# Performance work log

Hardware: AMD Instinct MI355X
Metric: run time of the kernel (lower is better)

The kernel has to match this reference:

```python
import jax, jax.numpy as jnp
import numpy as np

NB_STEPS = 50  # quadrature steps (51 Clenshaw-Curtis nodes)
IN_D = 8
HIDDEN = [256, 256, 256]
B = 8192


def _cc_quadrature(nb_steps):
    # Clenshaw-Curtis weights/nodes, exactly as in UMNN's ParallelNeuralIntegral
    lam = np.arange(nb_steps + 1).reshape(-1, 1)
    lam = np.cos((lam @ lam.T) * np.pi / nb_steps)
    lam[:, 0] = 0.5
    lam[:, -1] = 0.5 * lam[:, -1]
    lam = lam * 2.0 / nb_steps
    W = np.arange(nb_steps + 1).reshape(-1, 1)
    W[np.arange(1, nb_steps + 1, 2)] = 0
    W = 2.0 / (1 - W.astype(np.float64) ** 2)
    W[0] = 1.0
    W[np.arange(1, nb_steps + 1, 2)] = 0.0
    cc_weights = (lam.T @ W).astype(np.float32)  # [S+1, 1]
    steps = np.cos(np.arange(nb_steps + 1).reshape(-1, 1) * np.pi / nb_steps).astype(np.float32)  # [S+1,1]
    return jnp.asarray(cc_weights), jnp.asarray(steps)


def setup_inputs() -> dict:
    key = jax.random.key(0)
    ks = jax.random.split(key, 20)
    inp = {
        "x": jax.random.normal(ks[0], (B, 1), dtype=jnp.float32),
        "h": jax.random.normal(ks[1], (B, IN_D - 1), dtype=jnp.float32),
    }
    # integrand net: in_d -> 256 -> 256 -> 256 -> 1
    i_dims = [IN_D] + HIDDEN + [1]
    for li, (d0, d1) in enumerate(zip(i_dims, i_dims[1:])):
        scale = 1.0 / np.sqrt(d0)
        inp[f"iW{li}"] = jax.random.uniform(ks[2 + li], (d0, d1), jnp.float32, -scale, scale)
        inp[f"ib{li}"] = jax.random.uniform(ks[6 + li], (d1,), jnp.float32, -scale, scale)
    # h net: (in_d-1) -> 256 -> 256 -> 256 -> 2
    h_dims = [IN_D - 1] + HIDDEN + [2]
    for li, (d0, d1) in enumerate(zip(h_dims, h_dims[1:])):
        scale = 1.0 / np.sqrt(d0)
        inp[f"hW{li}"] = jax.random.uniform(ks[10 + li], (d0, d1), jnp.float32, -scale, scale)
        inp[f"hb{li}"] = jax.random.uniform(ks[14 + li], (d1,), jnp.float32, -scale, scale)
    return inp


def _integrand(z, Ws, bs):
    # IntegrandNN: Linear+ReLU chain, final Linear+ELU, then +1
    for W, b in zip(Ws[:-1], bs[:-1]):
        z = jax.nn.relu(z @ W + b)
    return jax.nn.elu(z @ Ws[-1] + bs[-1]) + 1.0


def _hnet(z, Ws, bs):
    # Linear+ReLU chain, final Linear (ReLU popped)
    for W, b in zip(Ws[:-1], bs[:-1]):
        z = jax.nn.relu(z @ W + b)
    return z @ Ws[-1] + bs[-1]


def _forward(x, h, iWs, ibs, hWs, hbs):
    cc_w, steps = _cc_quadrature(NB_STEPS)  # [S,1], [S,1]
    S = NB_STEPS + 1
    b = x.shape[0]
    # quadrature nodes mapped from [-1,1] to [0, x] (x0 = 0)
    X = x[:, None, :] * (steps[None, :, :] + 1.0) * 0.5          # [B,S,1]
    Hs = jnp.broadcast_to(h[:, None, :], (b, S, h.shape[1]))     # [B,S,in_d-1]
    z = jnp.concatenate([X, Hs], axis=-1)                        # [B,S,in_d]
    dz = _integrand(z, iWs, ibs)                                 # [B,S,1]
    integral = jnp.sum(dz * cc_w[None, :, :], axis=1) * x * 0.5  # [B,1]
    out = _hnet(h, hWs, hbs)                                     # [B,2]
    offset = out[:, :1]
    scaling = jnp.exp(out[:, 1:2])
    return scaling * integral + offset


def reference(x, h, iW0, ib0, iW1, ib1, iW2, ib2, iW3, ib3,
              hW0, hb0, hW1, hb1, hW2, hb2, hW3, hb3):
    iWs = [iW0, iW1, iW2, iW3]
    ibs = [ib0, ib1, ib2, ib3]
    hWs = [hW0, hW1, hW2, hW3]
    hbs = [hb0, hb1, hb2, hb3]
    return _forward(x, h, iWs, ibs, hWs, hbs)
```

## Files before the change

### kernel.cpp

```cpp
#include <hip/hip_runtime.h>
#include <hip/hip_bf16.h>
#include <math.h>

using bf16x8 = __attribute__((ext_vector_type(8))) __bf16;
using f32x4  = __attribute__((ext_vector_type(4))) float;

#define B_SZ    8192
#define S_STEPS 51
#define M_ROWS  (B_SZ * S_STEPS)
#define TROWS   128

__device__ __forceinline__ f32x4 mfma16(bf16x8 a, bf16x8 b, f32x4 c) {
    return __builtin_amdgcn_mfma_f32_16x16x32_bf16(a, b, c, 0, 0, 0);
}

__global__ void ccq_kernel(float* __restrict__ ccw, float* __restrict__ stp) {
    int s = threadIdx.x;
    if (s >= S_STEPS) return;
    double pi50 = M_PI / 50.0;
    double acc = 0.0;
    for (int j = 0; j <= 50; j += 2) {
        double wq = (j == 0) ? 1.0 : 2.0 / (1.0 - (double)(j * j));
        double m;
        if (s == 0) m = 0.5;
        else if (s == 50) m = 0.5;
        else m = cos((double)(j * s) * pi50);
        acc += m * wq;
    }
    ccw[s] = (float)(acc * (2.0 / 50.0));
    stp[s] = (float)cos((double)s * pi50);
}

struct PackArgs {
    const float* src[8];
    __hip_bfloat16* dst[8];
    int Ks[8], Ns[8], KST[8], perm[8];
    int prefix[9];
};

__global__ void pack_all(PackArgs pa) {
    int idx = blockIdx.x * 256 + threadIdx.x;
    if (idx >= pa.prefix[8]) return;
    int m = 0;
    while (idx >= pa.prefix[m + 1]) ++m;
    int e = idx - pa.prefix[m];
    int KSTEPS = pa.KST[m];
    int j    = e & 7;
    int lane = (e >> 3) & 63;
    int ks   = (e >> 9) % KSTEPS;
    int cg   = (e >> 9) / KSTEPS;
    int col = cg * 16 + (lane & 15);
    int k   = ks * 32 + (lane >> 4) * 8 + j;
    int kk  = pa.perm[m] ? ((k & ~31) + ((k & 31) >> 1) + (k & 1) * 16) : k;
    float v = (kk < pa.Ks[m] && col < pa.Ns[m]) ? pa.src[m][kk * pa.Ns[m] + col] : 0.0f;
    ((__bf16*)pa.dst[m])[e] = (__bf16)v;
}


template<int KSTEPS, int CHUNKS, int MASK>
__device__ __forceinline__ void gemm_compute(const __bf16* __restrict__ actIn,
                                             const __bf16* __restrict__ wpack,
                                             f32x4 (&acc)[4][4],
                                             int wr, int wc, int lane) {
    const bf16x8* wp = (const bf16x8*)wpack;
    const int la = lane & 15, hi = lane >> 4;

#pragma unroll
    for (int ks = 0; ks < KSTEPS; ++ks) {
        bf16x8 bbuf[4];
#pragma unroll
        for (int n = 0; n < 4; ++n)
            bbuf[n] = wp[((wc * 4 + n) * KSTEPS + ks) * 64 + lane];
#pragma unroll
        for (int m = 0; m < 4; ++m) {
            int row   = wr * 64 + m * 16 + la;
            int chunk = ks * 4 + hi;
            bf16x8 af = *(const bf16x8*)(actIn + (row * CHUNKS + (chunk ^ (row & MASK))) * 8);
#pragma unroll
            for (int n = 0; n < 4; ++n)
                acc[m][n] = mfma16(af, bbuf[n], acc[m][n]);
        }
    }
}

__device__ __forceinline__ void epilogue_store(f32x4 (&acc)[4][4],
                                               const float* __restrict__ bias,
                                               __bf16* __restrict__ actOut,
                                               int wr, int wc, int lane) {
    const int la = lane & 15, hi = lane >> 4;
    unsigned* dst = (unsigned*)actOut;
#pragma unroll
    for (int p = 0; p < 2; ++p) {
        int f0 = wc * 64 + p * 32 + la;
        float b0 = bias[f0], b1 = bias[f0 + 16];
        int kd = (wc * 2 + p) * 16 + la;
#pragma unroll
        for (int m = 0; m < 4; ++m) {
#pragma unroll
            for (int r = 0; r < 4; ++r) {
                int row = wr * 64 + m * 16 + hi * 4 + r;
                float v0 = fmaxf(acc[m][2 * p][r] + b0, 0.0f);
                float v1 = fmaxf(acc[m][2 * p + 1][r] + b1, 0.0f);
                union { __bf16 h[2]; unsigned u; } cv;
                cv.h[0] = (__bf16)v0; cv.h[1] = (__bf16)v1;
                dst[(row * 32 + ((kd >> 2) ^ (row & 7))) * 4 + (kd & 3)] = cv.u;
            }
        }
    }
}

template<int MODE>
__device__ __forceinline__ void final_layer(const __bf16* __restrict__ actIn,
                                            const __bf16* __restrict__ wpack,
                                            const float* __restrict__ bias,
                                            float* __restrict__ out0,
                                            float* __restrict__ out1,
                                            int rb, int wid, int lane) {
    const bf16x8* wp = (const bf16x8*)wpack;
    f32x4 acc = (f32x4)0.0f;
    for (int ks = 0; ks < 8; ++ks) {
        int row   = wid * 16 + (lane & 15);
        int chunk = ks * 4 + (lane >> 4);
        bf16x8 af = *(const bf16x8*)(actIn + (row * 32 + (chunk ^ (row & 7))) * 8);
        acc = mfma16(af, wp[ks * 64 + lane], acc);
    }
    int col = lane & 15;
    if (MODE == 0) {
        if (col == 0) {
            float b = bias[0];
#pragma unroll
            for (int r = 0; r < 4; ++r) {
                int row = wid * 16 + (lane >> 4) * 4 + r;
                float v = acc[r] + b;
                out0[rb + row] = (v > 0.0f) ? (v + 1.0f) : expf(v);
            }
        }
    } else {
        if (col < 2) {
            float b = bias[col];
            float* dst = (col == 0) ? out0 : out1;
#pragma unroll
            for (int r = 0; r < 4; ++r) {
                int row = wid * 16 + (lane >> 4) * 4 + r;
                dst[rb + row] = acc[r] + b;
            }
        }
    }
}

template<int MODE>
__global__ __launch_bounds__(512, 2) void mlp_kernel(
    const float* __restrict__ x, const float* __restrict__ h,
    const float* __restrict__ steps,
    const __bf16* __restrict__ w0p, const __bf16* __restrict__ w1p,
    const __bf16* __restrict__ w2p, const __bf16* __restrict__ w3p,
    const float* __restrict__ b0, const float* __restrict__ b1,
    const float* __restrict__ b2, const float* __restrict__ b3,
    float* __restrict__ out0, float* __restrict__ out1) {
    __shared__ __bf16 act[TROWS * 256];
    __shared__ __bf16 zin[TROWS * 32];

    int tid  = threadIdx.x;
    int lane = tid & 63;
    int wid  = tid >> 6;
    int wr   = wid >> 2;
    int wc   = wid & 3;
    int rb   = blockIdx.x * TROWS;

    {
        int row   = tid >> 2;
        int cpart = tid & 3;
        float vals[8];
        if (MODE == 0) {
            int s  = rb >> 13;
            int i  = (rb & (B_SZ - 1)) + row;
            float sc = (steps[s] + 1.0f) * 0.5f;
#pragma unroll
            for (int j = 0; j < 8; ++j) {
                int c = cpart * 8 + j;
                float v = 0.0f;
                if (c == 0) v = x[i] * sc;
                else if (c < 8) v = h[i * 7 + c - 1];
                vals[j] = v;
            }
        } else {
            int i = rb + row;
#pragma unroll
            for (int j = 0; j < 8; ++j) {
                int c = cpart * 8 + j;
                vals[j] = (c < 7) ? h[i * 7 + c] : 0.0f;
            }
        }
        bf16x8 zv;
#pragma unroll
        for (int j = 0; j < 8; ++j) zv[j] = (__bf16)vals[j];
        int zidx = (row * 4 + (cpart ^ (row & 3))) * 8;
        *(bf16x8*)(zin + zidx) = zv;
    }
    __syncthreads();

    f32x4 acc[4][4];

#pragma unroll
    for (int m = 0; m < 4; ++m)
#pragma unroll
        for (int n = 0; n < 4; ++n) acc[m][n] = (f32x4)0.0f;
    gemm_compute<1, 4, 3>(zin, w0p, acc, wr, wc, lane);
    epilogue_store(acc, b0, act, wr, wc, lane);
    __syncthreads();

#pragma unroll
    for (int m = 0; m < 4; ++m)
#pragma unroll
        for (int n = 0; n < 4; ++n) acc[m][n] = (f32x4)0.0f;
    gemm_compute<8, 32, 7>(act, w1p, acc, wr, wc, lane);
    __syncthreads();
    epilogue_store(acc, b1, act, wr, wc, lane);
    __syncthreads();

#pragma unroll
    for (int m = 0; m < 4; ++m)
#pragma unroll
        for (int n = 0; n < 4; ++n) acc[m][n] = (f32x4)0.0f;
    gemm_compute<8, 32, 7>(act, w2p, acc, wr, wc, lane);
    __syncthreads();
    epilogue_store(acc, b2, act, wr, wc, lane);
    __syncthreads();

    final_layer<MODE>(act, w3p, b3, out0, out1, rb, wid, lane);
}

__global__ void reduce_kernel(const float* __restrict__ dz, const float* __restrict__ x,
                              const float* __restrict__ ho, const float* __restrict__ hs,
                              const float* __restrict__ ccw, float* __restrict__ out) {
    __shared__ float w[S_STEPS];
    int t = threadIdx.x;
    if (t < S_STEPS) w[t] = ccw[t];
    __syncthreads();
    int i = blockIdx.x * blockDim.x + t;
    float acc = 0.0f;
    for (int s = 0; s < S_STEPS; ++s) acc += dz[s * B_SZ + i] * w[s];
    float integral = acc * x[i] * 0.5f;
    out[i] = expf(hs[i]) * integral + ho[i];
}

extern "C" void kernel_launch(void* const* d_in, const int* in_sizes, int n_in,
                              void* d_out, int out_size, void* d_ws, size_t ws_size,
                              hipStream_t stream) {
    (void)in_sizes; (void)n_in; (void)out_size; (void)ws_size;
    const float* x = (const float*)d_in[0];
    const float* h = (const float*)d_in[1];
    const float* iW[4] = {(const float*)d_in[2], (const float*)d_in[4],
                          (const float*)d_in[6], (const float*)d_in[8]};
    const float* ib[4] = {(const float*)d_in[3], (const float*)d_in[5],
                          (const float*)d_in[7], (const float*)d_in[9]};
    const float* hW[4] = {(const float*)d_in[10], (const float*)d_in[12],
                          (const float*)d_in[14], (const float*)d_in[16]};
    const float* hb[4] = {(const float*)d_in[11], (const float*)d_in[13],
                          (const float*)d_in[15], (const float*)d_in[17]};

    size_t off = 0;
    auto alloc = [&](size_t bytes) -> void* {
        void* p = (char*)d_ws + off;
        off += (bytes + 255) & ~(size_t)255;
        return p;
    };
    float*  dz   = (float*)alloc((size_t)M_ROWS * 4);
    float*  ho   = (float*)alloc(B_SZ * 4);
    float*  hs   = (float*)alloc(B_SZ * 4);
    float*  ccw  = (float*)alloc(64 * 4);
    float*  stp  = (float*)alloc(64 * 4);
    __bf16* iW0p = (__bf16*)alloc(16 * 1 * 512 * 2);
    __bf16* iW1p = (__bf16*)alloc(16 * 8 * 512 * 2);
    __bf16* iW2p = (__bf16*)alloc(16 * 8 * 512 * 2);
    __bf16* iW3p = (__bf16*)alloc(1 * 8 * 512 * 2);
    __bf16* hW0p = (__bf16*)alloc(16 * 1 * 512 * 2);
    __bf16* hW1p = (__bf16*)alloc(16 * 8 * 512 * 2);
    __bf16* hW2p = (__bf16*)alloc(16 * 8 * 512 * 2);
    __bf16* hW3p = (__bf16*)alloc(1 * 8 * 512 * 2);

    ccq_kernel<<<1, 64, 0, stream>>>(ccw, stp);

    PackArgs pa;
    const float* srcs[8] = {iW[0], iW[1], iW[2], iW[3], hW[0], hW[1], hW[2], hW[3]};
    __bf16*      dsts[8] = {iW0p, iW1p, iW2p, iW3p, hW0p, hW1p, hW2p, hW3p};
    int Ks[8]  = {8, 256, 256, 256, 7, 256, 256, 256};
    int Ns[8]  = {256, 256, 256, 1, 256, 256, 256, 2};
    int KST[8] = {1, 8, 8, 8, 1, 8, 8, 8};
    int CG[8]  = {16, 16, 16, 1, 16, 16, 16, 1};
    int PM[8]  = {0, 1, 1, 1, 0, 1, 1, 1};
    int pfx = 0;
    for (int m = 0; m < 8; ++m) {
        pa.src[m] = srcs[m];
        pa.dst[m] = (__hip_bfloat16*)dsts[m];
        pa.Ks[m] = Ks[m]; pa.Ns[m] = Ns[m]; pa.KST[m] = KST[m]; pa.perm[m] = PM[m];
        pa.prefix[m] = pfx;
        pfx += CG[m] * KST[m] * 512;
    }
    pa.prefix[8] = pfx;
    pack_all<<<(pfx + 255) / 256, 256, 0, stream>>>(pa);

    mlp_kernel<0><<<M_ROWS / TROWS, 512, 0, stream>>>(
        x, h, stp, iW0p, iW1p, iW2p, iW3p, ib[0], ib[1], ib[2], ib[3], dz, dz);
    mlp_kernel<1><<<B_SZ / TROWS, 512, 0, stream>>>(
        x, h, stp, hW0p, hW1p, hW2p, hW3p, hb[0], hb[1], hb[2], hb[3], ho, hs);

    reduce_kernel<<<B_SZ / 256, 256, 0, stream>>>(dz, x, ho, hs, ccw, (float*)d_out);
}
```

Before: 174.8 us.

## Switch MLP GEMMs to 32x32x16 MFMA with 64-row tiles and 4 waves

Replaces the 16x16x32 bf16 MFMA tiling with 32x32x16 MFMA and shrinks the row tile from 128 to 64 rows per block, using 256 threads instead of 512. Each wave now owns a 64x64 output tile as 2x2 32x32 accumulators. The weight packing, epilogue layout and final layer are reworked to match the new MFMA operand and accumulator layouts. The aim is fewer MFMA issues and a better instruction mix per output. In exchange, only two of the four waves do the final-layer work, and launch bounds change to allow four blocks per CU.

```diff
diff --git a/kernel.cpp b/kernel.cpp
--- a/kernel.cpp
+++ b/kernel.cpp
@@ -3,15 +3,15 @@
 #include <math.h>
 
 using bf16x8 = __attribute__((ext_vector_type(8))) __bf16;
-using f32x4  = __attribute__((ext_vector_type(4))) float;
+using f32x16 = __attribute__((ext_vector_type(16))) float;
 
 #define B_SZ    8192
 #define S_STEPS 51
 #define M_ROWS  (B_SZ * S_STEPS)
-#define TROWS   128
-
-__device__ __forceinline__ f32x4 mfma16(bf16x8 a, bf16x8 b, f32x4 c) {
-    return __builtin_amdgcn_mfma_f32_16x16x32_bf16(a, b, c, 0, 0, 0);
+#define TROWS   64
+
+__device__ __forceinline__ f32x16 mfma32(bf16x8 a, bf16x8 b, f32x16 c) {
+    return __builtin_amdgcn_mfma_f32_32x32x16_bf16(a, b, c, 0, 0, 0);
 }
 
 __global__ void ccq_kernel(float* __restrict__ ccw, float* __restrict__ stp) {
@@ -44,67 +44,61 @@
     int m = 0;
     while (idx >= pa.prefix[m + 1]) ++m;
     int e = idx - pa.prefix[m];
-    int KSTEPS = pa.KST[m];
+    int KST = pa.KST[m];
     int j    = e & 7;
     int lane = (e >> 3) & 63;
-    int ks   = (e >> 9) % KSTEPS;
-    int cg   = (e >> 9) / KSTEPS;
-    int col = cg * 16 + (lane & 15);
-    int k   = ks * 32 + (lane >> 4) * 8 + j;
-    int kk  = pa.perm[m] ? ((k & ~31) + ((k & 31) >> 1) + (k & 1) * 16) : k;
+    int ks   = (e >> 9) % KST;
+    int cg   = (e >> 9) / KST;
+    int col = cg * 32 + (lane & 31);
+    int k   = ks * 16 + (lane >> 5) * 8 + j;
+    int kk  = pa.perm[m] ? ((k & ~63) | (((k & 63) >> 1) + 32 * (k & 1))) : k;
     float v = (kk < pa.Ks[m] && col < pa.Ns[m]) ? pa.src[m][kk * pa.Ns[m] + col] : 0.0f;
     ((__bf16*)pa.dst[m])[e] = (__bf16)v;
 }
 
 
-template<int KSTEPS, int CHUNKS, int MASK>
+template<int KST, int CHUNKS, int MASK>
 __device__ __forceinline__ void gemm_compute(const __bf16* __restrict__ actIn,
                                              const __bf16* __restrict__ wpack,
-                                             f32x4 (&acc)[4][4],
-                                             int wr, int wc, int lane) {
+                                             f32x16 (&acc)[2][2],
+                                             int wc, int lane) {
     const bf16x8* wp = (const bf16x8*)wpack;
-    const int la = lane & 15, hi = lane >> 4;
-
-#pragma unroll
-    for (int ks = 0; ks < KSTEPS; ++ks) {
-        bf16x8 bbuf[4];
-#pragma unroll
-        for (int n = 0; n < 4; ++n)
-            bbuf[n] = wp[((wc * 4 + n) * KSTEPS + ks) * 64 + lane];
-#pragma unroll
-        for (int m = 0; m < 4; ++m) {
-            int row   = wr * 64 + m * 16 + la;
-            int chunk = ks * 4 + hi;
+    const int la = lane & 31, hi = lane >> 5;
+#pragma unroll 4
+    for (int ks = 0; ks < KST; ++ks) {
+        bf16x8 b0 = wp[((wc * 2 + 0) * KST + ks) * 64 + lane];
+        bf16x8 b1 = wp[((wc * 2 + 1) * KST + ks) * 64 + lane];
+        int chunk = ks * 2 + hi;
+#pragma unroll
+        for (int m = 0; m < 2; ++m) {
+            int row = m * 32 + la;
             bf16x8 af = *(const bf16x8*)(actIn + (row * CHUNKS + (chunk ^ (row & MASK))) * 8);
-#pragma unroll
-            for (int n = 0; n < 4; ++n)
-                acc[m][n] = mfma16(af, bbuf[n], acc[m][n]);
-        }
-    }
-}
-
-__device__ __forceinline__ void epilogue_store(f32x4 (&acc)[4][4],
+            acc[m][0] = mfma32(af, b0, acc[m][0]);
+            acc[m][1] = mfma32(af, b1, acc[m][1]);
+        }
+    }
+}
+
+__device__ __forceinline__ void epilogue_store(f32x16 (&acc)[2][2],
                                                const float* __restrict__ bias,
                                                __bf16* __restrict__ actOut,
-                                               int wr, int wc, int lane) {
-    const int la = lane & 15, hi = lane >> 4;
+                                               int wc, int lane) {
+    const int la = lane & 31, hi = lane >> 5;
     unsigned* dst = (unsigned*)actOut;
-#pragma unroll
-    for (int p = 0; p < 2; ++p) {
-        int f0 = wc * 64 + p * 32 + la;
-        float b0 = bias[f0], b1 = bias[f0 + 16];
-        int kd = (wc * 2 + p) * 16 + la;
-#pragma unroll
-        for (int m = 0; m < 4; ++m) {
-#pragma unroll
-            for (int r = 0; r < 4; ++r) {
-                int row = wr * 64 + m * 16 + hi * 4 + r;
-                float v0 = fmaxf(acc[m][2 * p][r] + b0, 0.0f);
-                float v1 = fmaxf(acc[m][2 * p + 1][r] + b1, 0.0f);
-                union { __bf16 h[2]; unsigned u; } cv;
-                cv.h[0] = (__bf16)v0; cv.h[1] = (__bf16)v1;
-                dst[(row * 32 + ((kd >> 2) ^ (row & 7))) * 4 + (kd & 3)] = cv.u;
-            }
+    int F = wc * 64 + la;
+    float b0 = bias[F], b1 = bias[F + 32];
+    int d = wc * 32 + la;
+    int c = d >> 2, w = d & 3;
+#pragma unroll
+    for (int m = 0; m < 2; ++m) {
+#pragma unroll
+        for (int r = 0; r < 16; ++r) {
+            int row = m * 32 + (r & 3) + 8 * (r >> 2) + 4 * hi;
+            float v0 = fmaxf(acc[m][0][r] + b0, 0.0f);
+            float v1 = fmaxf(acc[m][1][r] + b1, 0.0f);
+            union { __bf16 h2[2]; unsigned u; } cv;
+            cv.h2[0] = (__bf16)v0; cv.h2[1] = (__bf16)v1;
+            dst[(row * 32 + (c ^ (row & 7))) * 4 + w] = cv.u;
         }
     }
 }
@@ -117,39 +111,40 @@
                                             float* __restrict__ out1,
                                             int rb, int wid, int lane) {
     const bf16x8* wp = (const bf16x8*)wpack;
-    f32x4 acc = (f32x4)0.0f;
-    for (int ks = 0; ks < 8; ++ks) {
-        int row   = wid * 16 + (lane & 15);
-        int chunk = ks * 4 + (lane >> 4);
+    const int la = lane & 31, hi = lane >> 5;
+    f32x16 acc = (f32x16)0.0f;
+    int row = wid * 32 + la;
+#pragma unroll 4
+    for (int ks = 0; ks < 16; ++ks) {
+        int chunk = ks * 2 + hi;
         bf16x8 af = *(const bf16x8*)(actIn + (row * 32 + (chunk ^ (row & 7))) * 8);
-        acc = mfma16(af, wp[ks * 64 + lane], acc);
-    }
-    int col = lane & 15;
+        acc = mfma32(af, wp[ks * 64 + lane], acc);
+    }
     if (MODE == 0) {
-        if (col == 0) {
+        if (la == 0) {
             float b = bias[0];
 #pragma unroll
-            for (int r = 0; r < 4; ++r) {
-                int row = wid * 16 + (lane >> 4) * 4 + r;
+            for (int r = 0; r < 16; ++r) {
+                int rr = wid * 32 + (r & 3) + 8 * (r >> 2) + 4 * hi;
                 float v = acc[r] + b;
-                out0[rb + row] = (v > 0.0f) ? (v + 1.0f) : expf(v);
+                out0[rb + rr] = (v > 0.0f) ? (v + 1.0f) : expf(v);
             }
         }
     } else {
-        if (col < 2) {
-            float b = bias[col];
-            float* dst = (col == 0) ? out0 : out1;
-#pragma unroll
-            for (int r = 0; r < 4; ++r) {
-                int row = wid * 16 + (lane >> 4) * 4 + r;
-                dst[rb + row] = acc[r] + b;
+        if (la < 2) {
+            float b = bias[la];
+            float* dst = (la == 0) ? out0 : out1;
+#pragma unroll
+            for (int r = 0; r < 16; ++r) {
+                int rr = wid * 32 + (r & 3) + 8 * (r >> 2) + 4 * hi;
+                dst[rb + rr] = acc[r] + b;
             }
         }
     }
 }
 
 template<int MODE>
-__global__ __launch_bounds__(512, 2) void mlp_kernel(
+__global__ __launch_bounds__(256, 4) void mlp_kernel(
     const float* __restrict__ x, const float* __restrict__ h,
     const float* __restrict__ steps,
     const __bf16* __restrict__ w0p, const __bf16* __restrict__ w1p,
@@ -163,8 +158,7 @@
     int tid  = threadIdx.x;
     int lane = tid & 63;
     int wid  = tid >> 6;
-    int wr   = wid >> 2;
-    int wc   = wid & 3;
+    int wc   = wid;
     int rb   = blockIdx.x * TROWS;
 
     {
@@ -199,35 +193,36 @@
     }
     __syncthreads();
 
-    f32x4 acc[4][4];
-
-#pragma unroll
-    for (int m = 0; m < 4; ++m)
-#pragma unroll
-        for (int n = 0; n < 4; ++n) acc[m][n] = (f32x4)0.0f;
-    gemm_compute<1, 4, 3>(zin, w0p, acc, wr, wc, lane);
-    epilogue_store(acc, b0, act, wr, wc, lane);
-    __syncthreads();
-
-#pragma unroll
-    for (int m = 0; m < 4; ++m)
-#pragma unroll
-        for (int n = 0; n < 4; ++n) acc[m][n] = (f32x4)0.0f;
-    gemm_compute<8, 32, 7>(act, w1p, acc, wr, wc, lane);
-    __syncthreads();
-    epilogue_store(acc, b1, act, wr, wc, lane);
-    __syncthreads();
-
-#pragma unroll
-    for (int m = 0; m < 4; ++m)
-#pragma unroll
-        for (int n = 0; n < 4; ++n) acc[m][n] = (f32x4)0.0f;
-    gemm_compute<8, 32, 7>(act, w2p, acc, wr, wc, lane);
-    __syncthreads();
-    epilogue_store(acc, b2, act, wr, wc, lane);
-    __syncthreads();
-
-    final_layer<MODE>(act, w3p, b3, out0, out1, rb, wid, lane);
+    f32x16 acc[2][2];
+
+#pragma unroll
+    for (int m = 0; m < 2; ++m)
+#pragma unroll
+        for (int n = 0; n < 2; ++n) acc[m][n] = (f32x16)0.0f;
+    gemm_compute<2, 4, 3>(zin, w0p, acc, wc, lane);
+    epilogue_store(acc, b0, act, wc, lane);
+    __syncthreads();
+
+#pragma unroll
+    for (int m = 0; m < 2; ++m)
+#pragma unroll
+        for (int n = 0; n < 2; ++n) acc[m][n] = (f32x16)0.0f;
+    gemm_compute<16, 32, 7>(act, w1p, acc, wc, lane);
+    __syncthreads();
+    epilogue_store(acc, b1, act, wc, lane);
+    __syncthreads();
+
+#pragma unroll
+    for (int m = 0; m < 2; ++m)
+#pragma unroll
+        for (int n = 0; n < 2; ++n) acc[m][n] = (f32x16)0.0f;
+    gemm_compute<16, 32, 7>(act, w2p, acc, wc, lane);
+    __syncthreads();
+    epilogue_store(acc, b2, act, wc, lane);
+    __syncthreads();
+
+    if (wid < 2)
+        final_layer<MODE>(act, w3p, b3, out0, out1, rb, wid, lane);
 }
 
 __global__ void reduce_kernel(const float* __restrict__ dz, const float* __restrict__ x,
@@ -270,14 +265,14 @@
     float*  hs   = (float*)alloc(B_SZ * 4);
     float*  ccw  = (float*)alloc(64 * 4);
     float*  stp  = (float*)alloc(64 * 4);
-    __bf16* iW0p = (__bf16*)alloc(16 * 1 * 512 * 2);
-    __bf16* iW1p = (__bf16*)alloc(16 * 8 * 512 * 2);
-    __bf16* iW2p = (__bf16*)alloc(16 * 8 * 512 * 2);
-    __bf16* iW3p = (__bf16*)alloc(1 * 8 * 512 * 2);
-    __bf16* hW0p = (__bf16*)alloc(16 * 1 * 512 * 2);
-    __bf16* hW1p = (__bf16*)alloc(16 * 8 * 512 * 2);
-    __bf16* hW2p = (__bf16*)alloc(16 * 8 * 512 * 2);
-    __bf16* hW3p = (__bf16*)alloc(1 * 8 * 512 * 2);
+    __bf16* iW0p = (__bf16*)alloc(8 * 2 * 512 * 2);
+    __bf16* iW1p = (__bf16*)alloc(8 * 16 * 512 * 2);
+    __bf16* iW2p = (__bf16*)alloc(8 * 16 * 512 * 2);
+    __bf16* iW3p = (__bf16*)alloc(1 * 16 * 512 * 2);
+    __bf16* hW0p = (__bf16*)alloc(8 * 2 * 512 * 2);
+    __bf16* hW1p = (__bf16*)alloc(8 * 16 * 512 * 2);
+    __bf16* hW2p = (__bf16*)alloc(8 * 16 * 512 * 2);
+    __bf16* hW3p = (__bf16*)alloc(1 * 16 * 512 * 2);
 
     ccq_kernel<<<1, 64, 0, stream>>>(ccw, stp);
 
@@ -286,8 +281,8 @@
     __bf16*      dsts[8] = {iW0p, iW1p, iW2p, iW3p, hW0p, hW1p, hW2p, hW3p};
     int Ks[8]  = {8, 256, 256, 256, 7, 256, 256, 256};
     int Ns[8]  = {256, 256, 256, 1, 256, 256, 256, 2};
-    int KST[8] = {1, 8, 8, 8, 1, 8, 8, 8};
-    int CG[8]  = {16, 16, 16, 1, 16, 16, 16, 1};
+    int KST[8] = {2, 16, 16, 16, 2, 16, 16, 16};
+    int CG[8]  = {8, 8, 8, 1, 8, 8, 8, 1};
     int PM[8]  = {0, 1, 1, 1, 0, 1, 1, 1};
     int pfx = 0;
     for (int m = 0; m < 8; ++m) {
@@ -300,9 +295,9 @@
     pa.prefix[8] = pfx;
     pack_all<<<(pfx + 255) / 256, 256, 0, stream>>>(pa);
 
-    mlp_kernel<0><<<M_ROWS / TROWS, 512, 0, stream>>>(
+    mlp_kernel<0><<<M_ROWS / TROWS, 256, 0, stream>>>(
         x, h, stp, iW0p, iW1p, iW2p, iW3p, ib[0], ib[1], ib[2], ib[3], dz, dz);
-    mlp_kernel<1><<<B_SZ / TROWS, 512, 0, stream>>>(
+    mlp_kernel<1><<<B_SZ / TROWS, 256, 0, stream>>>(
         x, h, stp, hW0p, hW1p, hW2p, hW3p, hb[0], hb[1], hb[2], hb[3], ho, hs);
 
     reduce_kernel<<<B_SZ / 256, 256, 0, stream>>>(dz, x, ho, hs, ccw, (float*)d_out);
```

Result: faster. 158.8 us (-9.1%).
